# Kernel optimization log

Hardware: AMD Instinct MI355X
Metric: run time of the kernel (lower is better)

Reference implementation:

```python
import jax, jax.numpy as jnp
import numpy as np

B, N, K = 256, 1024, 64          # batch, atoms per structure, abc combinations
E = 2 * K                        # embedding_dim = 128
NSG = 230                        # number of space groups
LN_EPS = 1e-5


def setup_inputs() -> dict:
    key = jax.random.key(0)
    ks = jax.random.split(key, 12)
    xav = float(np.sqrt(6.0 / (K + K)))  # xavier_uniform bound for [K,K] slices
    return {
        "atom_positions": jax.random.uniform(ks[0], (B, N, 3), dtype=jnp.float32),
        "reciprocal_matrices": jax.random.normal(ks[1], (B, 3, 3), dtype=jnp.float32),
        "space_group": jax.random.randint(ks[2], (B, 1), 1, NSG + 1, dtype=jnp.int32),
        "abc_combinations": jax.random.normal(ks[3], (K, 3), dtype=jnp.float32),
        "graphs_array": jax.random.uniform(ks[4], (NSG, K, K), dtype=jnp.float32),
        "w_real": jax.random.uniform(ks[5], (NSG, K, K), jnp.float32, -xav, xav),
        "w_imag": jax.random.uniform(ks[6], (NSG, K, K), jnp.float32, -xav, xav),
        "b_real": jnp.zeros((NSG, K), jnp.float32),
        "b_imag": jnp.zeros((NSG, K), jnp.float32),
        "W2": jax.random.normal(ks[7], (E, E), dtype=jnp.float32) * 0.05,
        "b2": jnp.zeros((E,), jnp.float32),
        "gamma": jnp.ones((E,), jnp.float32),
        "beta": jnp.zeros((E,), jnp.float32),
    }


def reference(atom_positions, reciprocal_matrices, space_group, abc_combinations,
              graphs_array, w_real, w_imag, b_real, b_imag, W2, b2, gamma, beta):
    sg = space_group[:, 0] - 1                                  # [B] in [0,229]
    # transformed_abc = abc @ recip^T : [B,K,3]
    t_abc = jnp.einsum('kc,bdc->bkd', abc_combinations, reciprocal_matrices)
    # encodings = exp(i*2pi * pos @ t_abc^T) : [B,N,K] complex
    phase = (2.0 * jnp.pi) * jnp.einsum('bnc,bkc->bnk', atom_positions, t_abc)
    enc = jax.lax.complex(jnp.cos(phase), jnp.sin(phase))
    # per-sample adjacency gather + complex batched matmul
    adj = graphs_array[sg]                                      # [B,K,K]
    weighted = jnp.einsum('bnk,bkm->bnm', enc, adj.astype(enc.dtype))
    weighted = weighted[:, :, :K]                               # slice to embedding_dim//2
    # SpaceGroupDenseLayer: per-sample complex expert weights
    Wc = jax.lax.complex(w_real, w_imag)[sg]                    # [B,K,K]
    bc = jax.lax.complex(b_real, b_imag)[sg][:, None, :]        # [B,1,K]
    out_c = jnp.einsum('bni,bif->bnf', weighted, Wc) + bc       # [B,N,K] complex
    x = jnp.concatenate([out_c.real, out_c.imag], axis=-1)      # [B,N,2K]
    x = jax.nn.silu(x)
    x = x @ W2.T + b2                                           # Linear(E,E)
    mu = jnp.mean(x, axis=-1, keepdims=True)
    var = jnp.mean(jnp.square(x - mu), axis=-1, keepdims=True)
    return (x - mu) * jax.lax.rsqrt(var + LN_EPS) * gamma + beta
```

## Files before the change

kernel.cpp:

```cpp
#include <hip/hip_runtime.h>
#include <math.h>

#define BB 256
#define NN 1024
#define KK 64
#define EE 128
#define TM 64

typedef _Float16 half8 __attribute__((ext_vector_type(8)));
typedef __fp16 fp16x2 __attribute__((ext_vector_type(2)));
typedef float f32x4 __attribute__((ext_vector_type(4)));

__device__ __forceinline__ int swz(int row, int halfcol) {
    return (row * EE + halfcol) ^ ((row & 7) << 3);
}

__device__ __forceinline__ void gload_lds16(const void* g, void* l) {
    __builtin_amdgcn_global_load_lds(
        (const __attribute__((address_space(1))) unsigned int*)g,
        (__attribute__((address_space(3))) unsigned int*)l, 16, 0, 0);
}

__global__ __launch_bounds__(256) void prep_kernel(
    const float* __restrict__ recip,
    const int* __restrict__ space_group,
    const float* __restrict__ abc,
    const float* __restrict__ graphs,
    const float* __restrict__ w_real,
    const float* __restrict__ w_imag,
    const float* __restrict__ b_real,
    const float* __restrict__ b_imag,
    const float* __restrict__ W2,
    _Float16* __restrict__ Mt,
    float* __restrict__ bbout,
    float* __restrict__ tabcP,
    _Float16* __restrict__ W2h)
{
    const int b = blockIdx.x;
    const int t = threadIdx.x;
    const int sg = space_group[b] - 1;

    if (b < EE * EE / 256) {
        const int idx = b * 256 + t;
        W2h[idx] = (_Float16)W2[idx];
    }

    __shared__ float adjL[KK * KK];
    __shared__ float wrL[KK * KK];
    __shared__ float wiL[KK * KK];

    const float* adjG = graphs + (size_t)sg * KK * KK;
    const float* wrG  = w_real + (size_t)sg * KK * KK;
    const float* wiG  = w_imag + (size_t)sg * KK * KK;
    for (int idx = t; idx < KK * KK; idx += 256) {
        adjL[idx] = adjG[idx];
        wrL[idx]  = wrG[idx];
        wiL[idx]  = wiG[idx];
    }
    __syncthreads();

    const int i  = t >> 2;
    const int f0 = (t & 3) * 16;
    float cr[16], ci[16];
#pragma unroll
    for (int c = 0; c < 16; ++c) { cr[c] = 0.f; ci[c] = 0.f; }
    for (int k = 0; k < KK; ++k) {
        const float a = adjL[i * KK + k];
#pragma unroll
        for (int c = 0; c < 16; ++c) {
            cr[c] += a * wrL[k * KK + f0 + c];
            ci[c] += a * wiL[k * KK + f0 + c];
        }
    }
    _Float16* Mb = Mt + (size_t)b * EE * EE;
#pragma unroll
    for (int c = 0; c < 16; ++c) {
        const int f = f0 + c;
        Mb[f * EE + i]             = (_Float16)cr[c];
        Mb[f * EE + KK + i]        = (_Float16)(-ci[c]);
        Mb[(KK + f) * EE + i]      = (_Float16)ci[c];
        Mb[(KK + f) * EE + KK + i] = (_Float16)cr[c];
    }
    if (t < EE) {
        bbout[b * EE + t] = (t < KK) ? b_real[sg * KK + t] : b_imag[sg * KK + (t - KK)];
    }
    if (t < KK) {
        const float a0 = abc[t * 3 + 0], a1 = abc[t * 3 + 1], a2 = abc[t * 3 + 2];
        const float* R = recip + b * 9;
        float4 v;
        v.x = a0 * R[0] + a1 * R[1] + a2 * R[2];
        v.y = a0 * R[3] + a1 * R[4] + a2 * R[5];
        v.z = a0 * R[6] + a1 * R[7] + a2 * R[8];
        v.w = 0.f;
        *(float4*)&tabcP[((size_t)b * KK + t) * 4] = v;
    }
}

__global__ __launch_bounds__(256) void main_kernel(
    const float* __restrict__ pos,
    const _Float16* __restrict__ Mt,
    const float* __restrict__ bball,
    const float* __restrict__ tabcP,
    const _Float16* __restrict__ W2h,
    const float* __restrict__ b2,
    const float* __restrict__ gamma,
    const float* __restrict__ beta,
    float* __restrict__ out)
{
    const int d = blockIdx.x;
    const int j  = d >> 3;
    const int b  = (d & 7) * 32 + (j >> 4);
    const int n0 = (j & 15) * TM;
    const int t  = threadIdx.x;
    const int w    = t >> 6;
    const int lane = t & 63;
    const int ln15 = lane & 15;
    const int kg   = lane >> 4;

    __shared__ __align__(16) _Float16 Bt[EE * EE];
    __shared__ __align__(16) _Float16 X[TM * EE];

    {
        const char* srcM = (const char*)(Mt + (size_t)b * EE * EE);
#pragma unroll
        for (int i = 0; i < 8; ++i) {
            const int c16 = t + i * 256;
            const int row = c16 >> 4;
            const int sl  = c16 & 15;
            const int g   = row * 16 + (sl ^ (row & 7));
            gload_lds16(srcM + g * 16, (char*)Bt + c16 * 16);
        }
    }

    const int grow = n0 + w * 16 + ln15;
    const float* pr = pos + ((size_t)b * NN + grow) * 3;
    const float px = pr[0], py = pr[1], pz = pr[2];
    const float* tp = tabcP + (size_t)b * KK * 4;

    half8 afrag[4];
#pragma unroll
    for (int mq = 0; mq < 2; ++mq) {
        _Float16 cb[8], sb[8];
#pragma unroll
        for (int jj = 0; jj < 8; ++jj) {
            const int k = mq * 32 + kg * 8 + jj;
            const float4 tv = *(const float4*)&tp[k * 4];
            const float rev = px * tv.x + py * tv.y + pz * tv.z;
            const float fr  = __builtin_amdgcn_fractf(rev);
            sb[jj] = (_Float16)__builtin_amdgcn_sinf(fr);
            cb[jj] = (_Float16)__builtin_amdgcn_cosf(fr);
        }
        afrag[mq]     = *(half8*)cb;
        afrag[mq + 2] = *(half8*)sb;
    }
    __syncthreads();

    __builtin_amdgcn_s_setprio(1);
    f32x4 acc[8];
#pragma unroll
    for (int nt = 0; nt < 8; ++nt) {
        const int n = nt * 16 + ln15;
        f32x4 a = {0.f, 0.f, 0.f, 0.f};
#pragma unroll
        for (int kc = 0; kc < 4; ++kc) {
            const half8 bf = *(const half8*)&Bt[swz(n, kc * 32 + kg * 8)];
            a = __builtin_amdgcn_mfma_f32_16x16x32_f16(bf, afrag[kc], a, 0, 0, 0);
        }
        acc[nt] = a;
    }
    __builtin_amdgcn_s_setprio(0);
    __syncthreads();

    {
        const char* srcW = (const char*)W2h;
#pragma unroll
        for (int i = 0; i < 8; ++i) {
            const int c16 = t + i * 256;
            const int row = c16 >> 4;
            const int sl  = c16 & 15;
            const int g   = row * 16 + (sl ^ (row & 7));
            gload_lds16(srcW + g * 16, (char*)Bt + c16 * 16);
        }
    }

    {
        const int xrow = w * 16 + ln15;
        const float* bbp = bball + b * EE;
#pragma unroll
        for (int nt = 0; nt < 8; ++nt) {
            const int cb0 = nt * 16 + kg * 4;
            const float4 bb4 = *(const float4*)&bbp[cb0];
            float sv[4];
            sv[0] = acc[nt][0] + bb4.x;
            sv[1] = acc[nt][1] + bb4.y;
            sv[2] = acc[nt][2] + bb4.z;
            sv[3] = acc[nt][3] + bb4.w;
#pragma unroll
            for (int r2 = 0; r2 < 4; ++r2)
                sv[r2] = sv[r2] * __builtin_amdgcn_rcpf(1.f + __expf(-sv[r2]));
            const fp16x2 p0 = __builtin_amdgcn_cvt_pkrtz(sv[0], sv[1]);
            const fp16x2 p1 = __builtin_amdgcn_cvt_pkrtz(sv[2], sv[3]);
            uint2 u;
            u.x = __builtin_bit_cast(unsigned int, p0);
            u.y = __builtin_bit_cast(unsigned int, p1);
            *(uint2*)&X[swz(xrow, cb0)] = u;
        }
    }

    const int arow = w * 16 + ln15;
    half8 a2[4];
#pragma unroll
    for (int kc = 0; kc < 4; ++kc)
        a2[kc] = *(const half8*)&X[swz(arow, kc * 32 + kg * 8)];
    __syncthreads();

    __builtin_amdgcn_s_setprio(1);
    f32x4 acc2[8];
#pragma unroll
    for (int nt = 0; nt < 8; ++nt) {
        const int n = nt * 16 + ln15;
        f32x4 a = {0.f, 0.f, 0.f, 0.f};
#pragma unroll
        for (int kc = 0; kc < 4; ++kc) {
            const half8 bf = *(const half8*)&Bt[swz(n, kc * 32 + kg * 8)];
            a = __builtin_amdgcn_mfma_f32_16x16x32_f16(a2[kc], bf, a, 0, 0, 0);
        }
        acc2[nt] = a;
    }
    __builtin_amdgcn_s_setprio(0);

    float s[4] = {0.f, 0.f, 0.f, 0.f}, q[4] = {0.f, 0.f, 0.f, 0.f};
#pragma unroll
    for (int nt = 0; nt < 8; ++nt) {
        const int col = nt * 16 + ln15;
        const float b2v = b2[col];
#pragma unroll
        for (int r2 = 0; r2 < 4; ++r2) {
            const float v = acc2[nt][r2] + b2v;
            acc2[nt][r2] = v;
            s[r2] += v;
            q[r2] += v * v;
        }
    }
#pragma unroll
    for (int m = 1; m < 16; m <<= 1) {
#pragma unroll
        for (int r2 = 0; r2 < 4; ++r2) {
            s[r2] += __shfl_xor(s[r2], m);
            q[r2] += __shfl_xor(q[r2], m);
        }
    }
    const float inv = 1.f / EE;
    float mu[4], rs[4];
#pragma unroll
    for (int r2 = 0; r2 < 4; ++r2) {
        mu[r2] = s[r2] * inv;
        rs[r2] = __builtin_amdgcn_rsqf(fmaxf(q[r2] * inv - mu[r2] * mu[r2], 0.f) + 1e-5f);
    }
#pragma unroll
    for (int nt = 0; nt < 8; ++nt) {
        const int col = nt * 16 + ln15;
        const float g  = gamma[col];
        const float be = beta[col];
#pragma unroll
        for (int r2 = 0; r2 < 4; ++r2) {
            const int rr = w * 16 + kg * 4 + r2;
            out[((size_t)b * NN + n0 + rr) * EE + col] =
                (acc2[nt][r2] - mu[r2]) * rs[r2] * g + be;
        }
    }
}

extern "C" void kernel_launch(void* const* d_in, const int* in_sizes, int n_in,
                              void* d_out, int out_size, void* d_ws, size_t ws_size,
                              hipStream_t stream) {
    const float* pos    = (const float*)d_in[0];
    const float* recip  = (const float*)d_in[1];
    const int*   sgp    = (const int*)d_in[2];
    const float* abc    = (const float*)d_in[3];
    const float* graphs = (const float*)d_in[4];
    const float* wr     = (const float*)d_in[5];
    const float* wi     = (const float*)d_in[6];
    const float* br     = (const float*)d_in[7];
    const float* bi     = (const float*)d_in[8];
    const float* W2     = (const float*)d_in[9];
    const float* b2     = (const float*)d_in[10];
    const float* gm     = (const float*)d_in[11];
    const float* bt     = (const float*)d_in[12];
    float* out = (float*)d_out;

    char* ws = (char*)d_ws;
    _Float16* Mt    = (_Float16*)ws;
    char* p = ws + (size_t)BB * EE * EE * 2;
    _Float16* W2h   = (_Float16*)p;            p += EE * EE * 2;
    float*    bball = (float*)p;               p += (size_t)BB * EE * 4;
    float*    tabcP = (float*)p;

    hipLaunchKernelGGL(prep_kernel, dim3(BB), dim3(256), 0, stream,
                       recip, sgp, abc, graphs, wr, wi, br, bi, W2, Mt, bball, tabcP, W2h);
    hipLaunchKernelGGL(main_kernel, dim3(BB * NN / TM), dim3(256), 0, stream,
                       pos, Mt, bball, tabcP, W2h, b2, gm, bt, out);
}
```

Measured before the change: 66.50 us.

## Split W2 staging into K halves to alias X into shared Bt buffer

The separate X tile buffer is removed and X now lives in the upper half of the Bt shared buffer. W2 is loaded in two K-halves of 64 columns each with a 64-wide swizzle, and the second GEMM runs in two passes with an extra barrier and reload between them. Launch bounds request four blocks per CU. The aim is to cut LDS use per block so more blocks can be resident. The cost is more synchronisation and a serialized second load of W2.

```diff
diff --git a/kernel.cpp b/kernel.cpp
--- a/kernel.cpp
+++ b/kernel.cpp
@@ -13,6 +13,9 @@
 
 __device__ __forceinline__ int swz(int row, int halfcol) {
     return (row * EE + halfcol) ^ ((row & 7) << 3);
+}
+__device__ __forceinline__ int swz64(int row, int halfcol) {
+    return (row << 6) + (halfcol ^ ((row & 7) << 3));
 }
 
 __device__ __forceinline__ void gload_lds16(const void* g, void* l) {
@@ -96,7 +99,7 @@
     }
 }
 
-__global__ __launch_bounds__(256) void main_kernel(
+__global__ __launch_bounds__(256, 4) void main_kernel(
     const float* __restrict__ pos,
     const _Float16* __restrict__ Mt,
     const float* __restrict__ bball,
@@ -118,7 +121,7 @@
     const int kg   = lane >> 4;
 
     __shared__ __align__(16) _Float16 Bt[EE * EE];
-    __shared__ __align__(16) _Float16 X[TM * EE];
+    _Float16* X = Bt + (EE * EE) / 2;
 
     {
         const char* srcM = (const char*)(Mt + (size_t)b * EE * EE);
@@ -174,12 +177,12 @@
     {
         const char* srcW = (const char*)W2h;
 #pragma unroll
-        for (int i = 0; i < 8; ++i) {
-            const int c16 = t + i * 256;
-            const int row = c16 >> 4;
-            const int sl  = c16 & 15;
-            const int g   = row * 16 + (sl ^ (row & 7));
-            gload_lds16(srcW + g * 16, (char*)Bt + c16 * 16);
+        for (int i = 0; i < 4; ++i) {
+            const int c = t + i * 256;
+            const int n = c >> 3;
+            const int s = c & 7;
+            const int g = n * 16 + (s ^ (n & 7));
+            gload_lds16(srcW + g * 16, (char*)Bt + c * 16);
         }
     }
 
@@ -221,9 +224,37 @@
         const int n = nt * 16 + ln15;
         f32x4 a = {0.f, 0.f, 0.f, 0.f};
 #pragma unroll
-        for (int kc = 0; kc < 4; ++kc) {
-            const half8 bf = *(const half8*)&Bt[swz(n, kc * 32 + kg * 8)];
+        for (int kc = 0; kc < 2; ++kc) {
+            const half8 bf = *(const half8*)&Bt[swz64(n, kc * 32 + kg * 8)];
             a = __builtin_amdgcn_mfma_f32_16x16x32_f16(a2[kc], bf, a, 0, 0, 0);
+        }
+        acc2[nt] = a;
+    }
+    __builtin_amdgcn_s_setprio(0);
+    __syncthreads();
+
+    {
+        const char* srcW = (const char*)W2h;
+#pragma unroll
+        for (int i = 0; i < 4; ++i) {
+            const int c = t + i * 256;
+            const int n = c >> 3;
+            const int s = c & 7;
+            const int g = n * 16 + 8 + (s ^ (n & 7));
+            gload_lds16(srcW + g * 16, (char*)Bt + c * 16);
+        }
+    }
+    __syncthreads();
+
+    __builtin_amdgcn_s_setprio(1);
+#pragma unroll
+    for (int nt = 0; nt < 8; ++nt) {
+        const int n = nt * 16 + ln15;
+        f32x4 a = acc2[nt];
+#pragma unroll
+        for (int kc = 0; kc < 2; ++kc) {
+            const half8 bf = *(const half8*)&Bt[swz64(n, kc * 32 + kg * 8)];
+            a = __builtin_amdgcn_mfma_f32_16x16x32_f16(a2[2 + kc], bf, a, 0, 0, 0);
         }
         acc2[nt] = a;
     }
```

Result: faster. 63.06 us (median of 2 runs) (-5.2%).
